# Optimization experiments

Hardware: AMD Instinct MI355X
Metric: run time of the kernel (lower is better)

Reference implementation:

```python
import jax, jax.numpy as jnp
import numpy as np
from functools import partial

K_SPARSE = 50  # k_sparse passed as int to __init__
EPS = 1e-12    # numerical guard inside sqrt (diagonal zeros)


def setup_inputs() -> dict:
    key = jax.random.key(0)
    k1, k2, k3, k4 = jax.random.split(key, 4)
    B, n, D = 16, 1000, 128
    locs = jax.random.uniform(k1, (B, n, 2), dtype=jnp.float32)
    init_embeddings = jax.random.normal(k2, (B, n, D), dtype=jnp.float32)
    W = jax.random.normal(k3, (1, D), dtype=jnp.float32) * 0.1  # nn.Linear(1, D).weight.T
    b = jax.random.normal(k4, (D,), dtype=jnp.float32) * 0.1    # nn.Linear bias
    return {"locs": locs, "init_embeddings": init_embeddings, "W": W, "b": b}


def _sparsify(dist):
    """Per-node top-k nearest neighbors (no self loops).
    dist: [B, n, n] -> (neighbor_idx [B, n, k], edge_attr [B, n, k])."""
    B, n, _ = dist.shape
    # mask self loops with +inf so they are never selected
    diag = jnp.eye(n, dtype=bool)
    masked = jnp.where(diag[None, :, :], jnp.inf, dist)
    neg_vals, idx = jax.lax.top_k(-masked, K_SPARSE)  # k smallest distances
    return idx, -neg_vals


def reference(locs, init_embeddings, W, b):
    B, n, _ = locs.shape
    D = init_embeddings.shape[-1]
    k = K_SPARSE

    # pairwise Euclidean distance matrix [B, n, n]
    diff = locs[:, :, None, :] - locs[:, None, :, :]
    dist = jnp.sqrt(jnp.sum(diff * diff, axis=-1) + EPS)

    nbr_idx, edge_attr = _sparsify(dist)  # [B, n, k] each

    # PyG Batch: concatenate graphs with node-index offsets of index * n
    offsets = (jnp.arange(B, dtype=jnp.int32) * n)[:, None]            # [B, 1]
    src = jnp.broadcast_to(jnp.arange(n, dtype=jnp.int32)[:, None], (n, k))
    src = (src.reshape(1, n * k) + offsets).reshape(-1)                # [B*n*k]
    dst = (nbr_idx.reshape(B, n * k).astype(jnp.int32) + offsets).reshape(-1)
    edge_index = jnp.stack([src, dst], axis=0)                          # [2, B*n*k]

    # edge_embed: Linear(1, D) on scalar distances
    edge_emb = edge_attr.reshape(-1, 1) @ W + b                         # [B*n*k, D]

    x = init_embeddings.reshape(B * n, D)                               # batched node feats
    return x, edge_index, edge_emb
```

## Files before the change

kernel.cpp:

```cpp
#include <hip/hip_runtime.h>
#include <cstdint>
#include <cstddef>


namespace {

constexpr int kB  = 16;
constexpr int kN  = 1000;
constexpr int kD  = 128;
constexpr int kK  = 50;
constexpr int kCPL = 16;
constexpr int kNodesPerBlock = 4;
constexpr int kBlocksPerBatch = kN / kNodesPerBlock;

__device__ __forceinline__ double pack_key(float dd, int j) {
  const unsigned long long u =
      ((unsigned long long)__float_as_uint(dd) << 32) | (unsigned)j;
  return __longlong_as_double((long long)u);
}

__global__ __launch_bounds__(256)
void tsp_edge_kernel(const float* __restrict__ locs,
                     const float* __restrict__ init_emb,
                     const float* __restrict__ W,
                     const float* __restrict__ bias,
                     float* __restrict__ out)
{
#pragma clang fp contract(off)
  const int tid  = threadIdx.x;
  const int wave = tid >> 6;
  const int lane = tid & 63;
  const int blk  = blockIdx.x;
  const int b    = blk / kBlocksPerBatch;
  const int node_in_b = (blk % kBlocksPerBatch) * kNodesPerBlock + wave;
  const int node = b * kN + node_in_b;

  __shared__ float2 sloc[kN];
  {
    const float4* gl4 = reinterpret_cast<const float4*>(locs + (size_t)b * kN * 2);
    float4* sl4 = reinterpret_cast<float4*>(sloc);
    for (int t = tid; t < kN / 2; t += 256) sl4[t] = gl4[t];
  }
  __syncthreads();

  const float2 my = sloc[node_in_b];

  double key[kCPL];
#pragma unroll
  for (int s = 0; s < kCPL; ++s) {
    const int j = lane + (s << 6);
    const bool valid = (j < kN) && (j != node_in_b);
    const float2 pj = sloc[(j < kN) ? j : 0];
    const float dx = my.x - pj.x;
    const float dy = my.y - pj.y;
    const float d2 = dx * dx + dy * dy;
    float dd = sqrtf(d2 + 1e-12f);
    if (!valid) dd = INFINITY;
    key[s] = pack_key(dd, j);
  }

#pragma unroll
  for (int kk = 2; kk <= kCPL; kk <<= 1) {
#pragma unroll
    for (int jj = kk >> 1; jj > 0; jj >>= 1) {
#pragma unroll
      for (int i = 0; i < kCPL; ++i) {
        const int l2 = i ^ jj;
        if (l2 > i) {
          const double a  = key[i];
          const double c  = key[l2];
          const double lo = fmin(a, c);
          const double hi = fmax(a, c);
          if ((i & kk) == 0) { key[i] = lo; key[l2] = hi; }
          else               { key[i] = hi; key[l2] = lo; }
        }
      }
    }
  }

  constexpr size_t X_SZ    = (size_t)kB * kN * kD;
  constexpr size_t E_SZ    = (size_t)kB * kN * kK;
  constexpr size_t SRC_OFF = X_SZ;
  constexpr size_t DST_OFF = X_SZ + E_SZ;
  constexpr size_t EMB_OFF = X_SZ + 2 * E_SZ;

  const float2 wv = reinterpret_cast<const float2*>(W)[lane];
  const float2 bv = reinterpret_cast<const float2*>(bias)[lane];
  float* ebase = out + EMB_OFF + (size_t)node * (kK * kD);
  const int col2 = lane * 2;

  int res_j = 0;
  const double INFK = __builtin_inf();

#pragma unroll 1
  for (int r = 0; r < kK; ++r) {
    double m = key[0];
#pragma unroll
    for (int off = 32; off >= 1; off >>= 1)
      m = fmin(m, __shfl_xor(m, off, 64));

    const unsigned long long u = (unsigned long long)__double_as_longlong(m);
    const float dist = __uint_as_float((unsigned)(u >> 32));
    if (lane == r) res_j = (int)(u & 0xFFFFFFFFull);

    float2 v;
    v.x = dist * wv.x + bv.x;
    v.y = dist * wv.y + bv.y;
    *reinterpret_cast<float2*>(ebase + (size_t)r * kD + col2) = v;

    if (key[0] == m) {
#pragma unroll
      for (int s = 0; s < kCPL - 1; ++s) key[s] = key[s + 1];
      key[kCPL - 1] = INFK;
    }
  }

  {
    const float2* srcp = reinterpret_cast<const float2*>(init_emb + (size_t)node * kD);
    float2* dstp = reinterpret_cast<float2*>(out + (size_t)node * kD);
    dstp[lane] = srcp[lane];
  }

  if (lane < kK) {
    out[SRC_OFF + (size_t)node * kK + lane] = (float)node;
    out[DST_OFF + (size_t)node * kK + lane] = (float)(b * kN + res_j);
  }
}

}

extern "C" void kernel_launch(void* const* d_in, const int* in_sizes, int n_in,
                              void* d_out, int out_size, void* d_ws, size_t ws_size,
                              hipStream_t stream) {
  const float* locs = (const float*)d_in[0];
  const float* emb  = (const float*)d_in[1];
  const float* W    = (const float*)d_in[2];
  const float* bias = (const float*)d_in[3];
  float* out = (float*)d_out;

  dim3 grid(kB * kBlocksPerBatch);
  dim3 block(256);
  hipLaunchKernelGGL(tsp_edge_kernel, grid, block, 0, stream, locs, emb, W, bias, out);
}
```

Measured before the change: 468.9 us.

## Extract four nearest neighbors per wave reduction round via butterfly merge

The top-k selection loop now reduces sorted groups of four candidates across the wave with a bitonic-style butterfly merge. Each round pulls out four minima, so 13 reduction rounds replace 50. Each lane then drops the consumed heads of its sorted list with a count-based shift. The embedding copy and the source-index writes move before the selection so their stores can overlap the compute. This cuts shuffle latency per selected neighbor but adds more shuffles and min/max operations per round and more register pressure.

After: 476.1 us. Within noise of the previous version (+1.5%).

```diff
diff --git a/kernel.cpp b/kernel.cpp
--- a/kernel.cpp
+++ b/kernel.cpp
@@ -12,11 +12,21 @@
 constexpr int kCPL = 16;
 constexpr int kNodesPerBlock = 4;
 constexpr int kBlocksPerBatch = kN / kNodesPerBlock;
+constexpr int kFullRounds = 12;
 
 __device__ __forceinline__ double pack_key(float dd, int j) {
   const unsigned long long u =
       ((unsigned long long)__float_as_uint(dd) << 32) | (unsigned)j;
   return __longlong_as_double((long long)u);
+}
+
+__device__ __forceinline__ float key_dist(double k) {
+  const unsigned long long u = (unsigned long long)__double_as_longlong(k);
+  return __uint_as_float((unsigned)(u >> 32));
+}
+
+__device__ __forceinline__ int key_idx(double k) {
+  return (int)((unsigned long long)__double_as_longlong(k) & 0xFFFFFFFFull);
 }
 
 __global__ __launch_bounds__(256)
@@ -35,6 +45,21 @@
   const int node_in_b = (blk % kBlocksPerBatch) * kNodesPerBlock + wave;
   const int node = b * kN + node_in_b;
 
+  constexpr size_t X_SZ    = (size_t)kB * kN * kD;
+  constexpr size_t E_SZ    = (size_t)kB * kN * kK;
+  constexpr size_t SRC_OFF = X_SZ;
+  constexpr size_t DST_OFF = X_SZ + E_SZ;
+  constexpr size_t EMB_OFF = X_SZ + 2 * E_SZ;
+
+  {
+    const float2* srcp = reinterpret_cast<const float2*>(init_emb + (size_t)node * kD);
+    float2* dstp = reinterpret_cast<float2*>(out + (size_t)node * kD);
+    dstp[lane] = srcp[lane];
+  }
+  if (lane < kK) {
+    out[SRC_OFF + (size_t)node * kK + lane] = (float)node;
+  }
+
   __shared__ float2 sloc[kN];
   {
     const float4* gl4 = reinterpret_cast<const float4*>(locs + (size_t)b * kN * 2);
@@ -78,12 +103,6 @@
     }
   }
 
-  constexpr size_t X_SZ    = (size_t)kB * kN * kD;
-  constexpr size_t E_SZ    = (size_t)kB * kN * kK;
-  constexpr size_t SRC_OFF = X_SZ;
-  constexpr size_t DST_OFF = X_SZ + E_SZ;
-  constexpr size_t EMB_OFF = X_SZ + 2 * E_SZ;
-
   const float2 wv = reinterpret_cast<const float2*>(W)[lane];
   const float2 bv = reinterpret_cast<const float2*>(bias)[lane];
   float* ebase = out + EMB_OFF + (size_t)node * (kK * kD);
@@ -93,36 +112,95 @@
   const double INFK = __builtin_inf();
 
 #pragma unroll 1
-  for (int r = 0; r < kK; ++r) {
-    double m = key[0];
-#pragma unroll
-    for (int off = 32; off >= 1; off >>= 1)
-      m = fmin(m, __shfl_xor(m, off, 64));
-
-    const unsigned long long u = (unsigned long long)__double_as_longlong(m);
-    const float dist = __uint_as_float((unsigned)(u >> 32));
-    if (lane == r) res_j = (int)(u & 0xFFFFFFFFull);
-
+  for (int r = 0; r < kFullRounds; ++r) {
+    double m0 = key[0], m1 = key[1], m2 = key[2], m3 = key[3];
+#pragma unroll
+    for (int st = 1; st < 64; st <<= 1) {
+      const double t0 = __shfl_xor(m0, st, 64);
+      const double t1 = __shfl_xor(m1, st, 64);
+      const double t2 = __shfl_xor(m2, st, 64);
+      const double t3 = __shfl_xor(m3, st, 64);
+      const double c0 = fmin(m0, t3);
+      const double c1 = fmin(m1, t2);
+      const double c2 = fmin(m2, t1);
+      const double c3 = fmin(m3, t0);
+      const double d0 = fmin(c0, c2), d2 = fmax(c0, c2);
+      const double d1 = fmin(c1, c3), d3 = fmax(c1, c3);
+      m0 = fmin(d0, d1); m1 = fmax(d0, d1);
+      m2 = fmin(d2, d3); m3 = fmax(d2, d3);
+    }
+
+    const int r4 = 4 * r;
+    if (lane == r4    ) res_j = key_idx(m0);
+    if (lane == r4 + 1) res_j = key_idx(m1);
+    if (lane == r4 + 2) res_j = key_idx(m2);
+    if (lane == r4 + 3) res_j = key_idx(m3);
+
+    {
+      const float a0 = key_dist(m0), a1 = key_dist(m1);
+      const float a2 = key_dist(m2), a3 = key_dist(m3);
+      float* rp = ebase + (size_t)r4 * kD + col2;
+      float2 v;
+      v.x = a0 * wv.x + bv.x;  v.y = a0 * wv.y + bv.y;
+      *reinterpret_cast<float2*>(rp) = v;
+      v.x = a1 * wv.x + bv.x;  v.y = a1 * wv.y + bv.y;
+      *reinterpret_cast<float2*>(rp + kD) = v;
+      v.x = a2 * wv.x + bv.x;  v.y = a2 * wv.y + bv.y;
+      *reinterpret_cast<float2*>(rp + 2 * kD) = v;
+      v.x = a3 * wv.x + bv.x;  v.y = a3 * wv.y + bv.y;
+      *reinterpret_cast<float2*>(rp + 3 * kD) = v;
+    }
+
+    const double w3 = m3;
+    const int c = (key[0] <= w3 ? 1 : 0) + (key[1] <= w3 ? 1 : 0) +
+                  (key[2] <= w3 ? 1 : 0) + (key[3] <= w3 ? 1 : 0);
+    if (c & 4) {
+#pragma unroll
+      for (int s = 0; s < kCPL - 4; ++s) key[s] = key[s + 4];
+      key[12] = INFK; key[13] = INFK; key[14] = INFK; key[15] = INFK;
+    }
+    if (c & 2) {
+#pragma unroll
+      for (int s = 0; s < kCPL - 2; ++s) key[s] = key[s + 2];
+      key[14] = INFK; key[15] = INFK;
+    }
+    if (c & 1) {
+#pragma unroll
+      for (int s = 0; s < kCPL - 1; ++s) key[s] = key[s + 1];
+      key[15] = INFK;
+    }
+  }
+
+  {
+    double m0 = key[0], m1 = key[1], m2 = key[2], m3 = key[3];
+#pragma unroll
+    for (int st = 1; st < 64; st <<= 1) {
+      const double t0 = __shfl_xor(m0, st, 64);
+      const double t1 = __shfl_xor(m1, st, 64);
+      const double t2 = __shfl_xor(m2, st, 64);
+      const double t3 = __shfl_xor(m3, st, 64);
+      const double c0 = fmin(m0, t3);
+      const double c1 = fmin(m1, t2);
+      const double c2 = fmin(m2, t1);
+      const double c3 = fmin(m3, t0);
+      const double d0 = fmin(c0, c2), d2 = fmax(c0, c2);
+      const double d1 = fmin(c1, c3), d3 = fmax(c1, c3);
+      m0 = fmin(d0, d1); m1 = fmax(d0, d1);
+      m2 = fmin(d2, d3); m3 = fmax(d2, d3);
+    }
+    if (lane == 48) res_j = key_idx(m0);
+    if (lane == 49) res_j = key_idx(m1);
+
+    const float a0 = key_dist(m0), a1 = key_dist(m1);
+    float* rp = ebase + (size_t)48 * kD + col2;
     float2 v;
-    v.x = dist * wv.x + bv.x;
-    v.y = dist * wv.y + bv.y;
-    *reinterpret_cast<float2*>(ebase + (size_t)r * kD + col2) = v;
-
-    if (key[0] == m) {
-#pragma unroll
-      for (int s = 0; s < kCPL - 1; ++s) key[s] = key[s + 1];
-      key[kCPL - 1] = INFK;
-    }
-  }
-
-  {
-    const float2* srcp = reinterpret_cast<const float2*>(init_emb + (size_t)node * kD);
-    float2* dstp = reinterpret_cast<float2*>(out + (size_t)node * kD);
-    dstp[lane] = srcp[lane];
+    v.x = a0 * wv.x + bv.x;  v.y = a0 * wv.y + bv.y;
+    *reinterpret_cast<float2*>(rp) = v;
+    v.x = a1 * wv.x + bv.x;  v.y = a1 * wv.y + bv.y;
+    *reinterpret_cast<float2*>(rp + kD) = v;
   }
 
   if (lane < kK) {
-    out[SRC_OFF + (size_t)node * kK + lane] = (float)node;
     out[DST_OFF + (size_t)node * kK + lane] = (float)(b * kN + res_j);
   }
 }
```
